# Kernel optimization log

Hardware: AMD Instinct MI355X
Metric: run time of the kernel (lower is better)

## Reference

```python
import jax, jax.numpy as jnp
import numpy as np

N_NODES = 100000
N_EDGES = 1600000
IN_DIM, HID_DIM, OUT_DIM = 128, 64, 64
NEG_SLOPE = 0.2


def _gat_layer(h_in, src, dst, W, a_src, a_dst, b, n_nodes):
    # h: [N, F_out]
    h = h_in @ W.T
    alpha_src = h @ a_src  # [N]
    alpha_dst = h @ a_dst  # [N]
    # per-edge raw attention logits (edge j->i: src=j, dst=i)
    e = jax.nn.leaky_relu(alpha_src[src] + alpha_dst[dst], NEG_SLOPE)  # [E]
    # segment softmax over incoming edges of each dst node
    m = jax.ops.segment_max(e, dst, num_segments=n_nodes)
    ex = jnp.exp(e - m[dst])
    denom = jax.ops.segment_sum(ex, dst, num_segments=n_nodes)
    alpha = ex / denom[dst]  # [E], denom > 0 thanks to self-loops
    out = jax.ops.segment_sum(h[src] * alpha[:, None], dst, num_segments=n_nodes)
    return out + b


def setup_inputs() -> dict:
    key = jax.random.key(0)
    ks = jax.random.split(key, 12)
    x = jax.random.normal(ks[0], (N_NODES, IN_DIM), dtype=jnp.float32)
    edge_index = jax.random.randint(ks[1], (2, N_EDGES), 0, N_NODES)
    edge_attr = jax.random.normal(ks[2], (N_EDGES, 1), dtype=jnp.float32)
    s1 = 1.0 / np.sqrt(IN_DIM)
    s2 = 1.0 / np.sqrt(HID_DIM)
    W1 = jax.random.normal(ks[3], (HID_DIM, IN_DIM), dtype=jnp.float32) * s1
    att_src1 = jax.random.normal(ks[4], (HID_DIM,), dtype=jnp.float32) * s2
    att_dst1 = jax.random.normal(ks[5], (HID_DIM,), dtype=jnp.float32) * s2
    b1 = jnp.zeros((HID_DIM,), dtype=jnp.float32)
    W2 = jax.random.normal(ks[6], (OUT_DIM, HID_DIM), dtype=jnp.float32) * s2
    att_src2 = jax.random.normal(ks[7], (OUT_DIM,), dtype=jnp.float32) * s2
    att_dst2 = jax.random.normal(ks[8], (OUT_DIM,), dtype=jnp.float32) * s2
    b2 = jnp.zeros((OUT_DIM,), dtype=jnp.float32)
    return {"x": x, "edge_index": edge_index, "edge_attr": edge_attr,
            "W1": W1, "att_src1": att_src1, "att_dst1": att_dst1, "b1": b1,
            "W2": W2, "att_src2": att_src2, "att_dst2": att_dst2, "b2": b2}


def reference(x, edge_index, edge_attr, W1, att_src1, att_dst1, b1,
              W2, att_src2, att_dst2, b2):
    n = x.shape[0]
    # add self-loops (PyG GATConv default); edge_attr unused (edge_dim=None)
    loop = jnp.arange(n, dtype=edge_index.dtype)
    src = jnp.concatenate([edge_index[0], loop])
    dst = jnp.concatenate([edge_index[1], loop])
    h = _gat_layer(x, src, dst, W1, att_src1, att_dst1, b1, n)
    h = jax.nn.relu(h)
    h = _gat_layer(h, src, dst, W2, att_src2, att_dst2, b2, n)
    # global_mean_pool with batch=None -> mean over all nodes, shape [1, F]
    return jnp.mean(h, axis=0, keepdims=True)
```

## Files before the change

### kernel.cpp

```cpp
#include <hip/hip_runtime.h>

#define NEG_SLOPE 0.2f
#define BSHIFT 6
#define NBMAX 2048
#define BCAP 1408
#define CHUNK 4096

typedef __attribute__((ext_vector_type(8))) short short8;
typedef __attribute__((ext_vector_type(4))) float f32x4;

__device__ __forceinline__ unsigned short f2b(float x) {
    unsigned u = __float_as_uint(x);
    u += 0x7fff + ((u >> 16) & 1);
    return (unsigned short)(u >> 16);
}
__device__ __forceinline__ float b2f(unsigned short u) {
    return __uint_as_float((unsigned)u << 16);
}

__global__ __launch_bounds__(256) void hist_kernel(
    const int* __restrict__ ei, int* __restrict__ hist, int E, int NB)
{
    __shared__ int cnt[NBMAX];
    const int tid = threadIdx.x;
    for (int i = tid; i < NB; i += 256) cnt[i] = 0;
    __syncthreads();
    const int start = blockIdx.x * CHUNK;
    const int end = min(start + CHUNK, E);
    for (int i = start + tid; i < end; i += 256)
        atomicAdd(&cnt[ei[E + i] >> BSHIFT], 1);
    __syncthreads();
    for (int i = tid; i < NB; i += 256)
        hist[(size_t)blockIdx.x * NB + i] = cnt[i];
}

__global__ __launch_bounds__(256) void colscan_kernel(
    int* __restrict__ hist, int* __restrict__ btotal, int NB, int NBLK)
{
    const int b = blockIdx.x * 256 + threadIdx.x;
    if (b >= NB) return;
    int run = 0;
    int blk = 0;
    for (; blk + 8 <= NBLK; blk += 8) {
        int w[8];
        #pragma unroll
        for (int j = 0; j < 8; ++j) w[j] = hist[(size_t)(blk + j) * NB + b];
        #pragma unroll
        for (int j = 0; j < 8; ++j) {
            hist[(size_t)(blk + j) * NB + b] = run;
            run += w[j];
        }
    }
    for (; blk < NBLK; ++blk) {
        int w = hist[(size_t)blk * NB + b];
        hist[(size_t)blk * NB + b] = run;
        run += w;
    }
    btotal[b] = run;
}

__global__ __launch_bounds__(256) void scatter_kernel(
    const int* __restrict__ ei, const int* __restrict__ hist,
    int* __restrict__ binned, int E, int NB)
{
    __shared__ int base[NBMAX], cnt2[NBMAX];
    const int tid = threadIdx.x;
    for (int i = tid; i < NB; i += 256) {
        base[i] = hist[(size_t)blockIdx.x * NB + i];
        cnt2[i] = 0;
    }
    __syncthreads();
    const int start = blockIdx.x * CHUNK;
    const int end = min(start + CHUNK, E);
    for (int i = start + tid; i < end; i += 256) {
        int s = ei[i], d = ei[E + i];
        int b = d >> BSHIFT;
        int r = base[b] + atomicAdd(&cnt2[b], 1);
        if (r < BCAP) binned[(size_t)b * BCAP + r] = (s << BSHIFT) | (d & 63);
    }
}

__global__ __launch_bounds__(256) void bscan_kernel(
    const int* __restrict__ btotal, int* __restrict__ bbase, int NB)
{
    __shared__ int lds[256];
    const int t = threadIdx.x;
    int v[8]; int s = 0;
    #pragma unroll
    for (int j = 0; j < 8; ++j) {
        int i = t * 8 + j;
        v[j] = (i < NB) ? min(btotal[i], BCAP) : 0;
        s += v[j];
    }
    lds[t] = s;
    __syncthreads();
    #pragma unroll
    for (int off = 1; off < 256; off <<= 1) {
        int x = (t >= off) ? lds[t - off] : 0;
        __syncthreads();
        lds[t] += x;
        __syncthreads();
    }
    int excl = (t > 0) ? lds[t - 1] : 0;
    #pragma unroll
    for (int j = 0; j < 8; ++j) {
        int i = t * 8 + j;
        if (i < NB) { bbase[i] = excl + 64 * i; excl += v[j]; }
    }
}

__global__ __launch_bounds__(256) void bucket_csr_kernel(
    const int* __restrict__ binned, const int* __restrict__ btotal,
    const int* __restrict__ bbase, int* __restrict__ row_ptr,
    int* __restrict__ esrc, int N)
{
    __shared__ int ldeg[64];
    __shared__ int lcur[64];
    const int b = blockIdx.x;
    const int tid = threadIdx.x;
    const int node0 = b << BSHIFT;
    const int cnt = min(btotal[b], BCAP);
    const int base_e = bbase[b];
    const int* bp = binned + (size_t)b * BCAP;

    if (tid < 64) ldeg[tid] = (node0 + tid < N) ? 1 : 0;
    __syncthreads();
    for (int i = tid; i < cnt; i += 256)
        atomicAdd(&ldeg[bp[i] & 63], 1);
    __syncthreads();
    if (tid < 64) {
        int v = ldeg[tid];
        int inc = v;
        #pragma unroll
        for (int off = 1; off < 64; off <<= 1) {
            int t2 = __shfl_up(inc, off, 64);
            if (tid >= off) inc += t2;
        }
        int excl = inc - v;
        int node = node0 + tid;
        if (node <= N) row_ptr[node] = base_e + excl;
        if (node < N) {
            esrc[base_e + excl] = node;
            lcur[tid] = base_e + excl + 1;
        }
    }
    __syncthreads();
    for (int i = tid; i < cnt; i += 256) {
        int v = bp[i];
        int pos = atomicAdd(&lcur[v & 63], 1);
        esrc[pos] = v >> BSHIFT;
    }
}

template<int K, bool BF16IN>
__global__ __launch_bounds__(256) void gemm_attn_kernel(
    const void* __restrict__ in_v, const float* __restrict__ W,
    const float* __restrict__ a_src, const float* __restrict__ a_dst,
    unsigned short* __restrict__ hb, float* __restrict__ asrc,
    float* __restrict__ adst, int N)
{
    constexpr int LDK = K + 8;
    __shared__ unsigned short xb[64 * LDK];
    __shared__ unsigned short wb[64 * LDK];
    __shared__ float avs[64], avd[64];

    const int tid = threadIdx.x;
    const int node0 = blockIdx.x * 64;
    const int w = tid >> 6;
    const int lane = tid & 63;
    const int col = lane & 15;
    const int quad = lane >> 4;

    if (tid < 64) { avs[tid] = a_src[tid]; avd[tid] = a_dst[tid]; }

    for (int i = tid; i < 64 * (K / 4); i += 256) {
        int r = i / (K / 4), c = i % (K / 4);
        float4 v = *(const float4*)&W[(size_t)r * K + 4 * c];
        *(ushort4*)&wb[r * LDK + 4 * c] =
            make_ushort4(f2b(v.x), f2b(v.y), f2b(v.z), f2b(v.w));
    }
    if (BF16IN) {
        const unsigned short* in = (const unsigned short*)in_v;
        for (int i = tid; i < 64 * (K / 8); i += 256) {
            int r = i / (K / 8), c = i % (K / 8);
            int node = node0 + r;
            ulonglong2 v = (node < N)
                ? *(const ulonglong2*)&in[(size_t)node * K + 8 * c]
                : make_ulonglong2(0ull, 0ull);
            *(ulonglong2*)&xb[r * LDK + 8 * c] = v;
        }
    } else {
        const float* in = (const float*)in_v;
        for (int i = tid; i < 64 * (K / 4); i += 256) {
            int r = i / (K / 4), c = i % (K / 4);
            int node = node0 + r;
            float4 v = (node < N) ? *(const float4*)&in[(size_t)node * K + 4 * c]
                                  : make_float4(0.f, 0.f, 0.f, 0.f);
            *(ushort4*)&xb[r * LDK + 4 * c] =
                make_ushort4(f2b(v.x), f2b(v.y), f2b(v.z), f2b(v.w));
        }
    }
    __syncthreads();

    f32x4 acc[4] = {f32x4{0,0,0,0}, f32x4{0,0,0,0}, f32x4{0,0,0,0}, f32x4{0,0,0,0}};
    #pragma unroll
    for (int kc = 0; kc < K / 32; ++kc) {
        short8 a = *(const short8*)&xb[(16 * w + col) * LDK + kc * 32 + quad * 8];
        #pragma unroll
        for (int j = 0; j < 4; ++j) {
            short8 b = *(const short8*)&wb[(16 * j + col) * LDK + kc * 32 + quad * 8];
            acc[j] = __builtin_amdgcn_mfma_f32_16x16x32_bf16(a, b, acc[j], 0, 0, 0);
        }
    }

    #pragma unroll
    for (int r = 0; r < 4; ++r) {
        const int node = node0 + 16 * w + quad * 4 + r;
        const bool valid = node < N;
        float vs = 0.f, vd = 0.f;
        #pragma unroll
        for (int j = 0; j < 4; ++j) {
            float hv = acc[j][r];
            int f = 16 * j + col;
            if (valid) hb[(size_t)node * 64 + f] = f2b(hv);
            vs = fmaf(hv, avs[f], vs);
            vd = fmaf(hv, avd[f], vd);
        }
        #pragma unroll
        for (int off = 8; off >= 1; off >>= 1) {
            vs += __shfl_down(vs, off, 16);
            vd += __shfl_down(vd, off, 16);
        }
        if (col == 0 && valid) { asrc[node] = vs; adst[node] = vd; }
    }
}

__global__ __launch_bounds__(256) void aggregate_csr_kernel(
    const int* __restrict__ row_ptr, const int* __restrict__ esrc,
    const float* __restrict__ asrc, const float* __restrict__ adst,
    const unsigned short* __restrict__ hb, const float* __restrict__ bias,
    unsigned short* __restrict__ gb, int N, int do_relu)
{
    const int node = (int)((blockIdx.x * 256 + threadIdx.x) >> 4);
    const int lane = threadIdx.x & 15;
    if (node >= N) return;
    const int beg = row_ptr[node];
    const int end = row_ptr[node + 1];
    const float ad = adst[node];
    float a0 = 0.f, a1 = 0.f, a2 = 0.f, a3 = 0.f, wsum = 0.f;
    int p = beg;
    for (; p + 4 <= end; p += 4) {
        int s[4]; ushort4 r[4]; float l[4];
        #pragma unroll
        for (int j = 0; j < 4; ++j) s[j] = esrc[p + j];
        #pragma unroll
        for (int j = 0; j < 4; ++j)
            r[j] = *(const ushort4*)(hb + (size_t)s[j] * 64 + lane * 4);
        #pragma unroll
        for (int j = 0; j < 4; ++j) l[j] = asrc[s[j]] + ad;
        #pragma unroll
        for (int j = 0; j < 4; ++j) {
            float ll = (l[j] > 0.f) ? l[j] : NEG_SLOPE * l[j];
            float w = __expf(ll);
            wsum += w;
            a0 = fmaf(w, b2f(r[j].x), a0);
            a1 = fmaf(w, b2f(r[j].y), a1);
            a2 = fmaf(w, b2f(r[j].z), a2);
            a3 = fmaf(w, b2f(r[j].w), a3);
        }
    }
    for (; p < end; ++p) {
        int s = esrc[p];
        ushort4 r = *(const ushort4*)(hb + (size_t)s * 64 + lane * 4);
        float l = asrc[s] + ad;
        l = (l > 0.f) ? l : NEG_SLOPE * l;
        float w = __expf(l);
        wsum += w;
        a0 = fmaf(w, b2f(r.x), a0);
        a1 = fmaf(w, b2f(r.y), a1);
        a2 = fmaf(w, b2f(r.z), a2);
        a3 = fmaf(w, b2f(r.w), a3);
    }
    const float inv = 1.0f / wsum;
    float4 v = make_float4(a0 * inv, a1 * inv, a2 * inv, a3 * inv);
    if (bias) {
        v.x += bias[lane * 4 + 0]; v.y += bias[lane * 4 + 1];
        v.z += bias[lane * 4 + 2]; v.w += bias[lane * 4 + 3];
    }
    if (do_relu) {
        v.x = fmaxf(v.x, 0.f); v.y = fmaxf(v.y, 0.f);
        v.z = fmaxf(v.z, 0.f); v.w = fmaxf(v.w, 0.f);
    }
    *(ushort4*)&gb[(size_t)node * 64 + lane * 4] =
        make_ushort4(f2b(v.x), f2b(v.y), f2b(v.z), f2b(v.w));
}

__global__ __launch_bounds__(256) void pool_kernel(
    const unsigned short* __restrict__ gb, const float* __restrict__ b2,
    float* __restrict__ out, int N)
{
    __shared__ float red[256];
    const int f = threadIdx.x & 63;
    const int sub = threadIdx.x >> 6;
    float acc = 0.f;
    for (int n = blockIdx.x * 4 + sub; n < N; n += gridDim.x * 4)
        acc += b2f(gb[(size_t)n * 64 + f]);
    red[threadIdx.x] = acc;
    __syncthreads();
    if (threadIdx.x < 64) {
        float s = red[f] + red[64 + f] + red[128 + f] + red[192 + f];
        atomicAdd(out + f, s * (1.0f / (float)N));
        if (blockIdx.x == 0) atomicAdd(out + f, b2[f]);
    }
}

extern "C" void kernel_launch(void* const* d_in, const int* in_sizes, int n_in,
                              void* d_out, int out_size, void* d_ws, size_t ws_size,
                              hipStream_t stream) {
    const float* x   = (const float*)d_in[0];
    const int*   ei  = (const int*)d_in[1];
    const float* W1  = (const float*)d_in[3];
    const float* as1 = (const float*)d_in[4];
    const float* ad1 = (const float*)d_in[5];
    const float* b1  = (const float*)d_in[6];
    const float* W2  = (const float*)d_in[7];
    const float* as2 = (const float*)d_in[8];
    const float* ad2 = (const float*)d_in[9];
    const float* b2  = (const float*)d_in[10];
    float* out = (float*)d_out;

    const int N = in_sizes[0] / 128;
    const int E = in_sizes[1] / 2;
    const int Etot = E + N;
    const int NB = (N + 63) >> BSHIFT;
    const int NBLK = (E + CHUNK - 1) / CHUNK;

    auto align4 = [](size_t v) { return (v + 3) & ~(size_t)3; };
    float* ws    = (float*)d_ws;
    size_t off = 0;
    unsigned short* hb = (unsigned short*)(ws + off); off += align4((size_t)N * 32);
    unsigned short* gb = (unsigned short*)(ws + off); off += align4((size_t)N * 32);
    float* asrc  = ws + off; off += align4(N);
    float* adst  = ws + off; off += align4(N);
    int* row_ptr = (int*)(ws + off); off += align4(N + 1);
    int* btotal  = (int*)(ws + off); off += NBMAX;
    int* bbase   = (int*)(ws + off); off += NBMAX;
    int* hist    = (int*)(ws + off); off += align4((size_t)NBLK * NB);
    int* esrc    = (int*)(ws + off); off += align4(Etot);
    int* binned  = (int*)gb;

    const int gemm_blocks = (N + 63) / 64;
    const int agg_blocks  = (int)(((size_t)N * 16 + 255) / 256);

    hipMemsetAsync(out, 0, 64 * sizeof(float), stream);

    hist_kernel<<<NBLK, 256, 0, stream>>>(ei, hist, E, NB);
    colscan_kernel<<<(NB + 255) / 256, 256, 0, stream>>>(hist, btotal, NB, NBLK);
    scatter_kernel<<<NBLK, 256, 0, stream>>>(ei, hist, binned, E, NB);
    bscan_kernel<<<1, 256, 0, stream>>>(btotal, bbase, NB);
    bucket_csr_kernel<<<NB, 256, 0, stream>>>(binned, btotal, bbase, row_ptr, esrc, N);

    gemm_attn_kernel<128, false><<<gemm_blocks, 256, 0, stream>>>(
        x, W1, as1, ad1, hb, asrc, adst, N);
    aggregate_csr_kernel<<<agg_blocks, 256, 0, stream>>>(
        row_ptr, esrc, asrc, adst, hb, b1, gb, N, 1);

    gemm_attn_kernel<64, true><<<gemm_blocks, 256, 0, stream>>>(
        gb, W2, as2, ad2, hb, asrc, adst, N);
    aggregate_csr_kernel<<<agg_blocks, 256, 0, stream>>>(
        row_ptr, esrc, asrc, adst, hb, nullptr, gb, N, 0);

    pool_kernel<<<512, 256, 0, stream>>>(gb, b2, out, N);
}
```

Baseline: 301.8 us.

## Parallelize histogram column scan with wave shuffles, remap scatter blocks, unroll aggregation

The column scan over per-chunk histograms now assigns one 64-lane wavefront per bucket column and does a shuffle-based prefix scan, replacing the single-thread serial walk over all chunks. The scatter kernel remaps block IDs to chunks in an interleaved pattern so that concurrently running blocks work on chunks spread across the edge array, likely to change write locality into bucket bins. The aggregation loop is unrolled from 4 to 8 edges to raise memory-level parallelism on gathers. Costs are more registers in aggregation and more launched threads in colscan.

```diff
diff --git a/kernel.cpp b/kernel.cpp
--- a/kernel.cpp
+++ b/kernel.cpp
@@ -37,26 +37,24 @@
 __global__ __launch_bounds__(256) void colscan_kernel(
     int* __restrict__ hist, int* __restrict__ btotal, int NB, int NBLK)
 {
-    const int b = blockIdx.x * 256 + threadIdx.x;
-    if (b >= NB) return;
+    const int col = (int)((blockIdx.x * 256 + threadIdx.x) >> 6);
+    const int ln  = threadIdx.x & 63;
+    if (col >= NB) return;
     int run = 0;
-    int blk = 0;
-    for (; blk + 8 <= NBLK; blk += 8) {
-        int w[8];
-        #pragma unroll
-        for (int j = 0; j < 8; ++j) w[j] = hist[(size_t)(blk + j) * NB + b];
-        #pragma unroll
-        for (int j = 0; j < 8; ++j) {
-            hist[(size_t)(blk + j) * NB + b] = run;
-            run += w[j];
-        }
-    }
-    for (; blk < NBLK; ++blk) {
-        int w = hist[(size_t)blk * NB + b];
-        hist[(size_t)blk * NB + b] = run;
-        run += w;
-    }
-    btotal[b] = run;
+    for (int r0 = 0; r0 < NBLK; r0 += 64) {
+        const int r = r0 + ln;
+        const bool ok = (r < NBLK);
+        int v = ok ? hist[(size_t)r * NB + col] : 0;
+        int inc = v;
+        #pragma unroll
+        for (int off = 1; off < 64; off <<= 1) {
+            int x = __shfl_up(inc, off, 64);
+            if (ln >= off) inc += x;
+        }
+        if (ok) hist[(size_t)r * NB + col] = run + inc - v;
+        run += __shfl(inc, 63, 64);
+    }
+    if (ln == 0) btotal[col] = run;
 }
 
 __global__ __launch_bounds__(256) void scatter_kernel(
@@ -64,13 +62,18 @@
     int* __restrict__ binned, int E, int NB)
 {
     __shared__ int base[NBMAX], cnt2[NBMAX];
+    const int nblk = gridDim.x;
+    const int q = nblk >> 3, rr = nblk & 7;
+    const int x = blockIdx.x & 7, k = blockIdx.x >> 3;
+    const int chunk = ((x < rr) ? x * (q + 1) : rr * (q + 1) + (x - rr) * q) + k;
+
     const int tid = threadIdx.x;
     for (int i = tid; i < NB; i += 256) {
-        base[i] = hist[(size_t)blockIdx.x * NB + i];
+        base[i] = hist[(size_t)chunk * NB + i];
         cnt2[i] = 0;
     }
     __syncthreads();
-    const int start = blockIdx.x * CHUNK;
+    const int start = chunk * CHUNK;
     const int end = min(start + CHUNK, E);
     for (int i = start + tid; i < end; i += 256) {
         int s = ei[i], d = ei[E + i];
@@ -249,17 +252,17 @@
     const float ad = adst[node];
     float a0 = 0.f, a1 = 0.f, a2 = 0.f, a3 = 0.f, wsum = 0.f;
     int p = beg;
-    for (; p + 4 <= end; p += 4) {
-        int s[4]; ushort4 r[4]; float l[4];
-        #pragma unroll
-        for (int j = 0; j < 4; ++j) s[j] = esrc[p + j];
-        #pragma unroll
-        for (int j = 0; j < 4; ++j)
+    for (; p + 8 <= end; p += 8) {
+        int s[8]; ushort4 r[8]; float l[8];
+        #pragma unroll
+        for (int j = 0; j < 8; ++j) s[j] = esrc[p + j];
+        #pragma unroll
+        for (int j = 0; j < 8; ++j)
             r[j] = *(const ushort4*)(hb + (size_t)s[j] * 64 + lane * 4);
         #pragma unroll
-        for (int j = 0; j < 4; ++j) l[j] = asrc[s[j]] + ad;
-        #pragma unroll
-        for (int j = 0; j < 4; ++j) {
+        for (int j = 0; j < 8; ++j) l[j] = asrc[s[j]] + ad;
+        #pragma unroll
+        for (int j = 0; j < 8; ++j) {
             float ll = (l[j] > 0.f) ? l[j] : NEG_SLOPE * l[j];
             float w = __expf(ll);
             wsum += w;
@@ -355,7 +358,7 @@
     hipMemsetAsync(out, 0, 64 * sizeof(float), stream);
 
     hist_kernel<<<NBLK, 256, 0, stream>>>(ei, hist, E, NB);
-    colscan_kernel<<<(NB + 255) / 256, 256, 0, stream>>>(hist, btotal, NB, NBLK);
+    colscan_kernel<<<(NB * 64 + 255) / 256, 256, 0, stream>>>(hist, btotal, NB, NBLK);
     scatter_kernel<<<NBLK, 256, 0, stream>>>(ei, hist, binned, E, NB);
     bscan_kernel<<<1, 256, 0, stream>>>(btotal, bbase, NB);
     bucket_csr_kernel<<<NB, 256, 0, stream>>>(binned, btotal, bbase, row_ptr, esrc, N);
```

Result: faster. 289.0 us (-4.3%).
